# Optimization experiments

Hardware: AMD Instinct MI355X
Metric: run time of the kernel (lower is better)

The kernel has to match this reference:

```python
import jax, jax.numpy as jnp
import numpy as np

ALPHA = 0.15       # blend weight for merged mean vs center token
SIZE_DELTA = 0.0   # additive smoothing on cluster sizes


def setup_inputs() -> dict:
    key = jax.random.key(0)
    B, T, C = 8, 4096, 1024
    x = jax.random.normal(key, (B, T, C), dtype=jnp.float32)
    return {"x": x, "layer_idx": 0, "requested_r": 2048}


def reference(x, layer_idx, requested_r):
    B, T, C = x.shape
    K = max(1, T - int(requested_r))

    # token importance scores = squared L2 norm per token
    scores = jnp.sum(x * x, axis=-1)                      # [B, T]
    # CLS protection: force token 0 to be kept
    scores = scores.at[:, 0].set(jnp.finfo(scores.dtype).max)
    _, keep_idx = jax.lax.top_k(scores, K)                # [B, K]
    keep_idx = jnp.sort(keep_idx, axis=-1)

    # cosine nearest-kept-center assignment
    feat = x / (jnp.linalg.norm(x, axis=-1, keepdims=True) + 1e-12)  # [B, T, C]
    kept_feat = jnp.take_along_axis(feat, keep_idx[..., None], axis=1)  # [B, K, C]
    sim = jnp.einsum('bth,bkh->btk', feat, kept_feat)     # [B, T, K]
    assign_idx = jnp.argmax(sim, axis=-1)                 # [B, T]
    # force each kept center to self-assign (vectorized scatter,
    # replaces the original Python double for-loop with .item() syncs)
    b_idx = jnp.arange(B)[:, None]
    assign_idx = assign_idx.at[b_idx, keep_idx].set(jnp.arange(K)[None, :])

    # scatter-based size-weighted merge: segment mean over assigned tokens
    seg = (assign_idx + jnp.arange(B)[:, None] * K).reshape(-1)       # [B*T]
    sums = jax.ops.segment_sum(x.reshape(B * T, C), seg, num_segments=B * K)
    cnt = jax.ops.segment_sum(jnp.ones((B * T,), x.dtype), seg, num_segments=B * K)
    merged = (sums / (cnt[:, None] + SIZE_DELTA)).reshape(B, K, C)    # [B, K, C]

    x_kept = jnp.take_along_axis(x, keep_idx[..., None], axis=1)      # [B, K, C]
    out = (1.0 - ALPHA) * x_kept + ALPHA * merged
    return out
```

## Files before the change

kernel.cpp:

```cpp
#include <hip/hip_runtime.h>
#include <hip/hip_bf16.h>
#include <float.h>
#include <math.h>

constexpr int B_ = 8;
constexpr int T_ = 4096;
constexpr int C_ = 1024;
constexpr int K_ = 2048;
constexpr int MROWS = T_ - K_;

constexpr int BM = 128, BN = 128, BK = 32;
constexpr int NB = K_ / BN;
constexpr int NKS = C_ / BK;
constexpr float REFINE_DELTA = 4e-4f;

typedef _Float16 f16x8 __attribute__((ext_vector_type(8)));
typedef float    f32x4 __attribute__((ext_vector_type(4)));

__device__ __forceinline__ void gload16(const ushort* g, ushort* l) {
  __builtin_amdgcn_global_load_lds(
      (const __attribute__((address_space(1))) unsigned int*)g,
      (__attribute__((address_space(3))) unsigned int*)l, 16, 0, 0);
}

__global__ __launch_bounds__(256) void split_score_kernel(
    const float* __restrict__ x, ushort* __restrict__ xh,
    double* __restrict__ sd, float* __restrict__ rnorm)
{
  int lane = threadIdx.x & 63, wave = threadIdx.x >> 6;
  int row = blockIdx.x * 4 + wave;
  size_t base = (size_t)row * C_;
  double s = 0.0;
  #pragma unroll
  for (int j = 0; j < 4; j++) {
    int i4 = j * 256 + lane * 4;
    float4 v = *reinterpret_cast<const float4*>(&x[base + i4]);
    ushort4 h;
    { _Float16 a = (_Float16)v.x; h.x = *(ushort*)&a; }
    { _Float16 a = (_Float16)v.y; h.y = *(ushort*)&a; }
    { _Float16 a = (_Float16)v.z; h.z = *(ushort*)&a; }
    { _Float16 a = (_Float16)v.w; h.w = *(ushort*)&a; }
    *reinterpret_cast<ushort4*>(&xh[base + i4]) = h;
    s += (double)v.x * v.x + (double)v.y * v.y
       + (double)v.z * v.z + (double)v.w * v.w;
  }
  #pragma unroll
  for (int off = 32; off > 0; off >>= 1) s += __shfl_down(s, off);
  if (lane == 0) {
    sd[row] = s;
    rnorm[row] = (float)(1.0 / (sqrt(s) + 1e-12));
  }
}

__global__ __launch_bounds__(256) void rank_kernel(
    const double* __restrict__ sd, int* __restrict__ flag)
{
  int b = blockIdx.y;
  __shared__ double sh[T_];
  for (int i = threadIdx.x; i < T_; i += 256)
    sh[i] = (i == 0) ? DBL_MAX : sd[b * T_ + i];
  __syncthreads();
  int t = blockIdx.x * 128 + (threadIdx.x >> 1);
  int half = threadIdx.x & 1;
  double key = sh[t];
  int cnt = 0;
  int j0 = half * 2048;
  #pragma unroll 4
  for (int jj = 0; jj < 2048; jj++) {
    int j = j0 + jj;
    double sj = sh[j];
    cnt += (sj > key) || (sj == key && j < t);
  }
  cnt += __shfl_xor(cnt, 1);
  if (half == 0) flag[b * T_ + t] = (cnt < K_) ? 1 : 0;
}

__global__ __launch_bounds__(256) void select_kernel(
    const int* __restrict__ flag, int* __restrict__ keep_idx,
    int* __restrict__ drop_idx, int* __restrict__ assign)
{
  int b = blockIdx.x, tid = threadIdx.x;
  __shared__ int sums[256];
  int f[16], s = 0;
  int base = b * T_ + tid * 16;
  #pragma unroll
  for (int i = 0; i < 16; i++) { f[i] = flag[base + i]; s += f[i]; }
  sums[tid] = s;
  __syncthreads();
  for (int off = 1; off < 256; off <<= 1) {
    int v = 0;
    if (tid >= off) v = sums[tid - off];
    __syncthreads();
    if (tid >= off) sums[tid] += v;
    __syncthreads();
  }
  int run = (tid == 0) ? 0 : sums[tid - 1];
  #pragma unroll
  for (int i = 0; i < 16; i++) {
    int t = tid * 16 + i;
    if (f[i]) { keep_idx[b * K_ + run] = t; assign[b * T_ + t] = run; run++; }
    else drop_idx[b * MROWS + (t - run)] = t;
  }
}

__global__ void zero_kernel(int* __restrict__ cnt, int* __restrict__ nref)
{
  int i = blockIdx.x * 256 + threadIdx.x;
  if (i < B_ * K_) cnt[i] = 1;
  if (i == 0) *nref = 0;
}

__global__ __launch_bounds__(256) void mfma_argmax_kernel(
    const ushort* __restrict__ xh, const float* __restrict__ rnorm,
    const int* __restrict__ keep_idx, const int* __restrict__ drop_idx,
    float* __restrict__ pb, float* __restrict__ ps, int* __restrict__ pk)
{
  __shared__ __align__(16) ushort lds[3][2][4][128][8];

  int b  = blockIdx.z;
  int m0 = blockIdx.y * BM;
  int n0 = blockIdx.x * BN;
  int tid = threadIdx.x;
  int lane = tid & 63, wave = tid >> 6;
  int quad = lane >> 4, col = lane & 15;
  int wm = wave >> 1, wn = wave & 1;

  int srow = tid & 127;
  int sc8  = (tid >> 7) * 8;

  int dtok_s = drop_idx[b * MROWS + m0 + srow];
  const ushort* ga = xh + (size_t)(b * T_ + dtok_s) * C_;
  int ktok_s = keep_idx[b * K_ + n0 + srow];
  const ushort* gb = xh + (size_t)(b * T_ + ktok_s) * C_;

  int ldst = tid * 8;

  float scale[4]; int ncand[4];
  #pragma unroll
  for (int j = 0; j < 4; j++) {
    int nn = n0 + wn * 64 + j * 16 + col;
    ncand[j] = nn;
    scale[j] = rnorm[b * T_ + keep_idx[b * K_ + nn]];
  }

  f32x4 acc[4][4];
  #pragma unroll
  for (int i = 0; i < 4; i++)
    #pragma unroll
    for (int j = 0; j < 4; j++) acc[i][j] = (f32x4)0.f;

  auto issue = [&](int stg) {
    int k0 = stg * BK;
    ushort* base = &lds[stg % 3][0][0][0][0];
    gload16(ga + k0 + sc8,      base + ldst);
    gload16(ga + k0 + 16 + sc8, base + ldst + 2048);
    gload16(gb + k0 + sc8,      base + 4096 + ldst);
    gload16(gb + k0 + 16 + sc8, base + 4096 + ldst + 2048);
  };

  issue(0);
  issue(1);
  asm volatile("s_waitcnt vmcnt(4)" ::: "memory");
  __builtin_amdgcn_sched_barrier(0);
  __builtin_amdgcn_s_barrier();
  __builtin_amdgcn_sched_barrier(0);

  for (int ks = 0; ks < NKS; ks++) {
    int cur = ks % 3;
    if (ks <= NKS - 3) issue(ks + 2);

    f16x8 fa[4], fb[4];
    #pragma unroll
    for (int i = 0; i < 4; i++) {
      int row = wm * 64 + i * 16 + col;
      fa[i] = *reinterpret_cast<const f16x8*>(&lds[cur][0][quad][row][0]);
    }
    #pragma unroll
    for (int j = 0; j < 4; j++) {
      int row = wn * 64 + j * 16 + col;
      fb[j] = *reinterpret_cast<const f16x8*>(&lds[cur][1][quad][row][0]);
    }
    #pragma unroll
    for (int i = 0; i < 4; i++)
      #pragma unroll
      for (int j = 0; j < 4; j++)
        acc[i][j] = __builtin_amdgcn_mfma_f32_16x16x32_f16(fa[i], fb[j], acc[i][j], 0, 0, 0);

    if (ks <= NKS - 3) {
      asm volatile("s_waitcnt vmcnt(4)" ::: "memory");
    } else if (ks == NKS - 2) {
      asm volatile("s_waitcnt vmcnt(0)" ::: "memory");
    }
    __builtin_amdgcn_sched_barrier(0);
    if (ks < NKS - 1) {
      __builtin_amdgcn_s_barrier();
      __builtin_amdgcn_sched_barrier(0);
    }
  }

  float* redb   = (float*)(&lds[0][0][0][0][0]);
  float* redsec = redb + 256;
  int*   redk   = (int*)(redb + 512);

  #pragma unroll
  for (int i = 0; i < 4; i++) {
    #pragma unroll
    for (int r = 0; r < 4; r++) {
      float b1 = -FLT_MAX, b2 = -FLT_MAX; int k1 = 0;
      #pragma unroll
      for (int j = 0; j < 4; j++) {
        float v = acc[i][j][r] * scale[j];
        if (v > b1) { b2 = b1; b1 = v; k1 = ncand[j]; }
        else if (v > b2) b2 = v;
      }
      #pragma unroll
      for (int off = 1; off < 16; off <<= 1) {
        float ob1 = __shfl_xor(b1, off);
        float ob2 = __shfl_xor(b2, off);
        int   ok1 = __shfl_xor(k1, off);
        if (ob1 > b1 || (ob1 == b1 && ok1 < k1)) { b2 = fmaxf(b1, ob2); b1 = ob1; k1 = ok1; }
        else b2 = fmaxf(b2, ob1);
      }
      if (col == 0) {
        int tl = wm * 64 + i * 16 + quad * 4 + r;
        redb[wn * 128 + tl] = b1; redsec[wn * 128 + tl] = b2; redk[wn * 128 + tl] = k1;
      }
    }
  }
  __syncthreads();
  if (tid < 128) {
    float b1 = redb[tid], b2 = redsec[tid]; int k1 = redk[tid];
    float o1 = redb[128 + tid], o2 = redsec[128 + tid]; int ok = redk[128 + tid];
    if (o1 > b1) { b2 = fmaxf(b1, o2); b1 = o1; k1 = ok; }
    else b2 = fmaxf(b2, o1);
    size_t p = ((size_t)(b * NB + blockIdx.x)) * MROWS + m0 + tid;
    pb[p] = b1; ps[p] = b2; pk[p] = k1;
  }
}

__global__ __launch_bounds__(256) void reduce2_kernel(
    const float* __restrict__ pb, const float* __restrict__ ps, const int* __restrict__ pk,
    const float* __restrict__ rnorm, const int* __restrict__ drop_idx,
    int* __restrict__ assign, int* __restrict__ cnt,
    int* __restrict__ rlist, int* __restrict__ nref)
{
  int idx2 = blockIdx.x * 256 + threadIdx.x;
  int b = idx2 >> 11;
  int rc = idx2 & (MROWS - 1);
  float b1 = -FLT_MAX, b2 = -FLT_MAX; int k1 = 0;
  for (int nb = 0; nb < NB; nb++) {
    size_t p = ((size_t)(b * NB + nb)) * MROWS + rc;
    float v = pb[p], s = ps[p]; int k = pk[p];
    if (v > b1) { b2 = fmaxf(b1, s); b1 = v; k1 = k; }
    else b2 = fmaxf(b2, v);
  }
  int t = drop_idx[idx2];
  assign[b * T_ + t] = k1;
  atomicAdd(&cnt[b * K_ + k1], 1);
  if ((b1 - b2) * rnorm[b * T_ + t] < REFINE_DELTA) {
    int qi = atomicAdd(nref, 1);
    rlist[qi] = idx2;
  }
}

__global__ __launch_bounds__(256) void refine_kernel(
    const float* __restrict__ x, const double* __restrict__ sd,
    const int* __restrict__ keep_idx, const int* __restrict__ drop_idx,
    const float* __restrict__ rnorm,
    const float* __restrict__ pb, const float* __restrict__ ps, const int* __restrict__ pk,
    const int* __restrict__ nref, const int* __restrict__ rlist,
    int* __restrict__ assign, int* __restrict__ cnt)
{
  __shared__ __align__(16) float xs[C_];
  __shared__ int cand[K_];
  __shared__ int ncand_s;
  __shared__ double wv[4];
  __shared__ int wk[4];
  __shared__ float spb[NB], sps[NB];
  __shared__ int spk[NB];
  int n = *nref;
  int lane = threadIdx.x & 63, wave = threadIdx.x >> 6;
  for (int qi = blockIdx.x; qi < n; qi += gridDim.x) {
    int idx2 = rlist[qi];
    int b = idx2 >> 11, rc = idx2 & (MROWS - 1);
    int t = drop_idx[idx2];
    int bt = b * T_ + t;
    __syncthreads();
    const float* xt = x + ((size_t)b * T_ + t) * C_;
    for (int i = threadIdx.x; i < C_; i += 256) xs[i] = xt[i];
    if (threadIdx.x < NB) {
      size_t p = ((size_t)(b * NB + threadIdx.x)) * MROWS + rc;
      spb[threadIdx.x] = pb[p]; sps[threadIdx.x] = ps[p]; spk[threadIdx.x] = pk[p];
    }
    __syncthreads();
    if (threadIdx.x == 0) {
      float b1 = -FLT_MAX;
      for (int nb = 0; nb < NB; nb++) if (spb[nb] > b1) b1 = spb[nb];
      float thr = b1 - REFINE_DELTA / rnorm[bt];
      int nc = 0;
      for (int nb = 0; nb < NB; nb++) {
        if (spb[nb] >= thr) {
          if (sps[nb] >= thr) { for (int j = 0; j < BN; j++) cand[nc++] = nb * BN + j; }
          else cand[nc++] = spk[nb];
        }
      }
      ncand_s = nc;
    }
    __syncthreads();
    int nc = ncand_s;
    double bv = -DBL_MAX; int bk = 0x7fffffff;
    for (int ci = wave; ci < nc; ci += 4) {
      int k = cand[ci];
      int kt = keep_idx[b * K_ + k];
      const float* xr = x + ((size_t)b * T_ + kt) * C_;
      double s = 0.0;
      int c0 = lane * 16;
      #pragma unroll
      for (int c = 0; c < 16; c += 4) {
        float4 v = *reinterpret_cast<const float4*>(&xr[c0 + c]);
        s += (double)xs[c0 + c]     * v.x + (double)xs[c0 + c + 1] * v.y
           + (double)xs[c0 + c + 2] * v.z + (double)xs[c0 + c + 3] * v.w;
      }
      #pragma unroll
      for (int off = 32; off > 0; off >>= 1) s += __shfl_down(s, off);
      s = __shfl(s, 0);
      s /= sqrt(sd[b * T_ + kt]);
      if (s > bv || (s == bv && k < bk)) { bv = s; bk = k; }
    }
    if (lane == 0) { wv[wave] = bv; wk[wave] = bk; }
    __syncthreads();
    if (threadIdx.x == 0) {
      double fb = wv[0]; int fk = wk[0];
      for (int w2 = 1; w2 < 4; w2++)
        if (wv[w2] > fb || (wv[w2] == fb && wk[w2] < fk)) { fb = wv[w2]; fk = wk[w2]; }
      int old = assign[bt];
      if (fk != old) {
        atomicSub(&cnt[b * K_ + old], 1);
        atomicAdd(&cnt[b * K_ + fk], 1);
        assign[bt] = fk;
      }
    }
  }
}

__global__ __launch_bounds__(256) void scan_kernel(
    const int* __restrict__ cnt, int* __restrict__ offs, int* __restrict__ cursor)
{
  int b = blockIdx.x, tid = threadIdx.x;
  __shared__ int sums[256];
  int v[8], s = 0;
  int base = b * K_ + tid * 8;
  #pragma unroll
  for (int i = 0; i < 8; i++) { v[i] = cnt[base + i]; s += v[i]; }
  sums[tid] = s;
  __syncthreads();
  for (int off = 1; off < 256; off <<= 1) {
    int t2 = 0;
    if (tid >= off) t2 = sums[tid - off];
    __syncthreads();
    if (tid >= off) sums[tid] += t2;
    __syncthreads();
  }
  int run = (tid == 0) ? 0 : sums[tid - 1];
  #pragma unroll
  for (int i = 0; i < 8; i++) { offs[base + i] = run; cursor[base + i] = run; run += v[i]; }
}

__global__ void scatter_kernel(const int* __restrict__ assign,
                               int* __restrict__ cursor, int* __restrict__ lists)
{
  int i = blockIdx.x * 256 + threadIdx.x;
  int b = i >> 12, t = i & (T_ - 1);
  int p = atomicAdd(&cursor[b * K_ + assign[i]], 1);
  lists[b * T_ + p] = t;
}

__global__ __launch_bounds__(256) void merge_kernel(
    const float* __restrict__ x, const int* __restrict__ keep_idx,
    const int* __restrict__ cnt, const int* __restrict__ offs,
    const int* __restrict__ lists, float* __restrict__ out)
{
  __shared__ int toks[256];
  int b = blockIdx.y, k = blockIdx.x;
  int m = cnt[b * K_ + k], off = offs[b * K_ + k];
  const float* xb = x + (size_t)b * T_ * C_;
  int c4 = threadIdx.x * 4;
  float sx = 0.f, sy = 0.f, sz = 0.f, sw = 0.f;
  for (int basei = 0; basei < m; basei += 256) {
    int nchunk = min(256, m - basei);
    __syncthreads();
    if (threadIdx.x < nchunk) toks[threadIdx.x] = lists[b * T_ + off + basei + threadIdx.x];
    __syncthreads();
    for (int i = 0; i < nchunk; i++) {
      int tok = toks[i];
      float4 v = *reinterpret_cast<const float4*>(&xb[(size_t)tok * C_ + c4]);
      sx += v.x; sy += v.y; sz += v.z; sw += v.w;
    }
  }
  int kt = keep_idx[b * K_ + k];
  float4 xk = *reinterpret_cast<const float4*>(&xb[(size_t)kt * C_ + c4]);
  float fm = (float)m;
  float4 o;
  o.x = 0.85f * xk.x + 0.15f * (sx / fm);
  o.y = 0.85f * xk.y + 0.15f * (sy / fm);
  o.z = 0.85f * xk.z + 0.15f * (sz / fm);
  o.w = 0.85f * xk.w + 0.15f * (sw / fm);
  *reinterpret_cast<float4*>(&out[((size_t)b * K_ + k) * C_ + c4]) = o;
}

extern "C" void kernel_launch(void* const* d_in, const int* in_sizes, int n_in,
                              void* d_out, int out_size, void* d_ws, size_t ws_size,
                              hipStream_t stream)
{
  const float* x = (const float*)d_in[0];
  float* out = (float*)d_out;

  char* w = (char*)d_ws;
  ushort* xh    = (ushort*)w;  w += sizeof(ushort) * (size_t)B_ * T_ * C_;
  float* pb     = (float*)w;   w += sizeof(float) * (size_t)B_ * NB * MROWS;
  float* ps     = (float*)w;   w += sizeof(float) * (size_t)B_ * NB * MROWS;
  int*   pk     = (int*)w;     w += sizeof(int) * (size_t)B_ * NB * MROWS;
  double* sd    = (double*)w;  w += sizeof(double) * B_ * T_;
  float* rnorm  = (float*)w;   w += sizeof(float) * B_ * T_;
  int* flag     = (int*)w;     w += sizeof(int) * B_ * T_;
  int* keep_idx = (int*)w;     w += sizeof(int) * B_ * K_;
  int* drop_idx = (int*)w;     w += sizeof(int) * B_ * MROWS;
  int* assign   = (int*)w;     w += sizeof(int) * B_ * T_;
  int* cnt      = (int*)w;     w += sizeof(int) * B_ * K_;
  int* offs     = (int*)w;     w += sizeof(int) * B_ * K_;
  int* cursor   = (int*)w;     w += sizeof(int) * B_ * K_;
  int* lists    = (int*)w;     w += sizeof(int) * B_ * T_;
  int* rlist    = (int*)w;     w += sizeof(int) * B_ * MROWS;
  int* nref     = (int*)w;     w += 256;

  split_score_kernel<<<B_ * T_ / 4, 256, 0, stream>>>(x, xh, sd, rnorm);
  rank_kernel<<<dim3(T_ / 128, B_), 256, 0, stream>>>(sd, flag);
  select_kernel<<<B_, 256, 0, stream>>>(flag, keep_idx, drop_idx, assign);
  zero_kernel<<<(B_ * K_ + 255) / 256, 256, 0, stream>>>(cnt, nref);
  mfma_argmax_kernel<<<dim3(NB, MROWS / BM, B_), 256, 0, stream>>>(
      xh, rnorm, keep_idx, drop_idx, pb, ps, pk);
  reduce2_kernel<<<B_ * MROWS / 256, 256, 0, stream>>>(
      pb, ps, pk, rnorm, drop_idx, assign, cnt, rlist, nref);
  refine_kernel<<<256, 256, 0, stream>>>(
      x, sd, keep_idx, drop_idx, rnorm, pb, ps, pk, nref, rlist, assign, cnt);
  scan_kernel<<<B_, 256, 0, stream>>>(cnt, offs, cursor);
  scatter_kernel<<<B_ * T_ / 256, 256, 0, stream>>>(assign, cursor, lists);
  merge_kernel<<<dim3(K_, B_), 256, 0, stream>>>(x, keep_idx, cnt, offs, lists, out);
}
```

Before: 558.0 us.

## Enlarge MFMA argmax tiles to 256x256, spread rank work wider, fuse zero init

The similarity GEMM now uses 256x256x64 tiles, 512 threads and 8 waves, with double buffering in place of the triple buffer and manual waitcnt. Each wave computes 128x64 outputs, which gives more operand reuse per LDS load and halves the partial-argmax columns that reduce2 reads. The rank kernel now splits each token's comparison over 16 lanes to get more parallel blocks, and the zero init moves into select_kernel, removing one launch. Risks: double buffering with __syncthreads may expose load latency, higher register and LDS use cuts occupancy, and the grid shrinks to 8x8x8 = 512 blocks.

```diff
diff --git a/kernel.cpp b/kernel.cpp
--- a/kernel.cpp
+++ b/kernel.cpp
@@ -9,7 +9,7 @@
 constexpr int K_ = 2048;
 constexpr int MROWS = T_ - K_;
 
-constexpr int BM = 128, BN = 128, BK = 32;
+constexpr int BM = 256, BN = 256, BK = 64;
 constexpr int NB = K_ / BN;
 constexpr int NKS = C_ / BK;
 constexpr float REFINE_DELTA = 4e-4f;
@@ -60,24 +60,28 @@
   for (int i = threadIdx.x; i < T_; i += 256)
     sh[i] = (i == 0) ? DBL_MAX : sd[b * T_ + i];
   __syncthreads();
-  int t = blockIdx.x * 128 + (threadIdx.x >> 1);
-  int half = threadIdx.x & 1;
+  int tt = threadIdx.x >> 4;
+  int g  = threadIdx.x & 15;
+  int t  = blockIdx.x * 16 + tt;
   double key = sh[t];
   int cnt = 0;
-  int j0 = half * 2048;
   #pragma unroll 4
-  for (int jj = 0; jj < 2048; jj++) {
-    int j = j0 + jj;
+  for (int jj = 0; jj < 256; jj++) {
+    int j = jj * 16 + g;
     double sj = sh[j];
     cnt += (sj > key) || (sj == key && j < t);
   }
   cnt += __shfl_xor(cnt, 1);
-  if (half == 0) flag[b * T_ + t] = (cnt < K_) ? 1 : 0;
+  cnt += __shfl_xor(cnt, 2);
+  cnt += __shfl_xor(cnt, 4);
+  cnt += __shfl_xor(cnt, 8);
+  if (g == 0) flag[b * T_ + t] = (cnt < K_) ? 1 : 0;
 }
 
 __global__ __launch_bounds__(256) void select_kernel(
     const int* __restrict__ flag, int* __restrict__ keep_idx,
-    int* __restrict__ drop_idx, int* __restrict__ assign)
+    int* __restrict__ drop_idx, int* __restrict__ assign,
+    int* __restrict__ cnt, int* __restrict__ nref)
 {
   int b = blockIdx.x, tid = threadIdx.x;
   __shared__ int sums[256];
@@ -101,40 +105,34 @@
     if (f[i]) { keep_idx[b * K_ + run] = t; assign[b * T_ + t] = run; run++; }
     else drop_idx[b * MROWS + (t - run)] = t;
   }
-}
-
-__global__ void zero_kernel(int* __restrict__ cnt, int* __restrict__ nref)
-{
-  int i = blockIdx.x * 256 + threadIdx.x;
-  if (i < B_ * K_) cnt[i] = 1;
-  if (i == 0) *nref = 0;
-}
-
-__global__ __launch_bounds__(256) void mfma_argmax_kernel(
+  #pragma unroll
+  for (int i = 0; i < 8; i++) cnt[b * K_ + tid * 8 + i] = 1;
+  if (b == 0 && tid == 0) *nref = 0;
+}
+
+__global__ __launch_bounds__(512) void mfma_argmax_kernel(
     const ushort* __restrict__ xh, const float* __restrict__ rnorm,
     const int* __restrict__ keep_idx, const int* __restrict__ drop_idx,
     float* __restrict__ pb, float* __restrict__ ps, int* __restrict__ pk)
 {
-  __shared__ __align__(16) ushort lds[3][2][4][128][8];
+  __shared__ __align__(16) ushort lds[2][2][8][256][8];
 
   int b  = blockIdx.z;
   int m0 = blockIdx.y * BM;
   int n0 = blockIdx.x * BN;
   int tid = threadIdx.x;
-  int lane = tid & 63, wave = tid >> 6;
+  int lane = tid & 63, w = tid >> 6;
   int quad = lane >> 4, col = lane & 15;
-  int wm = wave >> 1, wn = wave & 1;
-
-  int srow = tid & 127;
-  int sc8  = (tid >> 7) * 8;
-
+  int wm = w >> 2, wn = w & 3;
+
+  int rg = w & 3;
+  int cb = (w >> 2) * 4;
+  int srow = rg * 64 + lane;
   int dtok_s = drop_idx[b * MROWS + m0 + srow];
   const ushort* ga = xh + (size_t)(b * T_ + dtok_s) * C_;
   int ktok_s = keep_idx[b * K_ + n0 + srow];
   const ushort* gb = xh + (size_t)(b * T_ + ktok_s) * C_;
 
-  int ldst = tid * 8;
-
   float scale[4]; int ncand[4];
   #pragma unroll
   for (int j = 0; j < 4; j++) {
@@ -143,67 +141,54 @@
     scale[j] = rnorm[b * T_ + keep_idx[b * K_ + nn]];
   }
 
-  f32x4 acc[4][4];
-  #pragma unroll
-  for (int i = 0; i < 4; i++)
+  f32x4 acc[8][4];
+  #pragma unroll
+  for (int i = 0; i < 8; i++)
     #pragma unroll
     for (int j = 0; j < 4; j++) acc[i][j] = (f32x4)0.f;
 
-  auto issue = [&](int stg) {
-    int k0 = stg * BK;
-    ushort* base = &lds[stg % 3][0][0][0][0];
-    gload16(ga + k0 + sc8,      base + ldst);
-    gload16(ga + k0 + 16 + sc8, base + ldst + 2048);
-    gload16(gb + k0 + sc8,      base + 4096 + ldst);
-    gload16(gb + k0 + 16 + sc8, base + 4096 + ldst + 2048);
+  auto issue = [&](int ks, int st) {
+    int k0 = ks * BK;
+    #pragma unroll
+    for (int c = 0; c < 4; c++) {
+      int ch = cb + c;
+      gload16(ga + k0 + ch * 8, &lds[st][0][ch][srow][0]);
+      gload16(gb + k0 + ch * 8, &lds[st][1][ch][srow][0]);
+    }
   };
 
-  issue(0);
-  issue(1);
-  asm volatile("s_waitcnt vmcnt(4)" ::: "memory");
-  __builtin_amdgcn_sched_barrier(0);
-  __builtin_amdgcn_s_barrier();
-  __builtin_amdgcn_sched_barrier(0);
+  issue(0, 0);
+  __syncthreads();
 
   for (int ks = 0; ks < NKS; ks++) {
-    int cur = ks % 3;
-    if (ks <= NKS - 3) issue(ks + 2);
-
-    f16x8 fa[4], fb[4];
+    int cur = ks & 1;
+    if (ks < NKS - 1) issue(ks + 1, cur ^ 1);
+
     #pragma unroll
-    for (int i = 0; i < 4; i++) {
-      int row = wm * 64 + i * 16 + col;
-      fa[i] = *reinterpret_cast<const f16x8*>(&lds[cur][0][quad][row][0]);
-    }
-    #pragma unroll
-    for (int j = 0; j < 4; j++) {
-      int row = wn * 64 + j * 16 + col;
-      fb[j] = *reinterpret_cast<const f16x8*>(&lds[cur][1][quad][row][0]);
-    }
-    #pragma unroll
-    for (int i = 0; i < 4; i++)
+    for (int s = 0; s < 2; s++) {
+      f16x8 fb[4];
       #pragma unroll
       for (int j = 0; j < 4; j++)
-        acc[i][j] = __builtin_amdgcn_mfma_f32_16x16x32_f16(fa[i], fb[j], acc[i][j], 0, 0, 0);
-
-    if (ks <= NKS - 3) {
-      asm volatile("s_waitcnt vmcnt(4)" ::: "memory");
-    } else if (ks == NKS - 2) {
-      asm volatile("s_waitcnt vmcnt(0)" ::: "memory");
-    }
-    __builtin_amdgcn_sched_barrier(0);
-    if (ks < NKS - 1) {
-      __builtin_amdgcn_s_barrier();
-      __builtin_amdgcn_sched_barrier(0);
-    }
+        fb[j] = *reinterpret_cast<const f16x8*>(
+            &lds[cur][1][s * 4 + quad][wn * 64 + j * 16 + col][0]);
+      #pragma unroll
+      for (int i = 0; i < 8; i++) {
+        f16x8 fa = *reinterpret_cast<const f16x8*>(
+            &lds[cur][0][s * 4 + quad][wm * 128 + i * 16 + col][0]);
+        #pragma unroll
+        for (int j = 0; j < 4; j++)
+          acc[i][j] = __builtin_amdgcn_mfma_f32_16x16x32_f16(fa, fb[j], acc[i][j], 0, 0, 0);
+      }
+    }
+    __syncthreads();
   }
 
   float* redb   = (float*)(&lds[0][0][0][0][0]);
-  float* redsec = redb + 256;
-  int*   redk   = (int*)(redb + 512);
-
-  #pragma unroll
-  for (int i = 0; i < 4; i++) {
+  float* redsec = redb + 1024;
+  int*   redk   = (int*)(redb + 2048);
+
+  #pragma unroll
+  for (int i = 0; i < 8; i++) {
     #pragma unroll
     for (int r = 0; r < 4; r++) {
       float b1 = -FLT_MAX, b2 = -FLT_MAX; int k1 = 0;
@@ -222,17 +207,20 @@
         else b2 = fmaxf(b2, ob1);
       }
       if (col == 0) {
-        int tl = wm * 64 + i * 16 + quad * 4 + r;
-        redb[wn * 128 + tl] = b1; redsec[wn * 128 + tl] = b2; redk[wn * 128 + tl] = k1;
+        int tl = wm * 128 + i * 16 + quad * 4 + r;
+        redb[wn * 256 + tl] = b1; redsec[wn * 256 + tl] = b2; redk[wn * 256 + tl] = k1;
       }
     }
   }
   __syncthreads();
-  if (tid < 128) {
+  if (tid < 256) {
     float b1 = redb[tid], b2 = redsec[tid]; int k1 = redk[tid];
-    float o1 = redb[128 + tid], o2 = redsec[128 + tid]; int ok = redk[128 + tid];
-    if (o1 > b1) { b2 = fmaxf(b1, o2); b1 = o1; k1 = ok; }
-    else b2 = fmaxf(b2, o1);
+    #pragma unroll
+    for (int q = 1; q < 4; q++) {
+      float o1 = redb[q * 256 + tid], o2 = redsec[q * 256 + tid]; int ok = redk[q * 256 + tid];
+      if (o1 > b1) { b2 = fmaxf(b1, o2); b1 = o1; k1 = ok; }
+      else b2 = fmaxf(b2, o1);
+    }
     size_t p = ((size_t)(b * NB + blockIdx.x)) * MROWS + m0 + tid;
     pb[p] = b1; ps[p] = b2; pk[p] = k1;
   }
@@ -434,10 +422,9 @@
   int* nref     = (int*)w;     w += 256;
 
   split_score_kernel<<<B_ * T_ / 4, 256, 0, stream>>>(x, xh, sd, rnorm);
-  rank_kernel<<<dim3(T_ / 128, B_), 256, 0, stream>>>(sd, flag);
-  select_kernel<<<B_, 256, 0, stream>>>(flag, keep_idx, drop_idx, assign);
-  zero_kernel<<<(B_ * K_ + 255) / 256, 256, 0, stream>>>(cnt, nref);
-  mfma_argmax_kernel<<<dim3(NB, MROWS / BM, B_), 256, 0, stream>>>(
+  rank_kernel<<<dim3(T_ / 16, B_), 256, 0, stream>>>(sd, flag);
+  select_kernel<<<B_, 256, 0, stream>>>(flag, keep_idx, drop_idx, assign, cnt, nref);
+  mfma_argmax_kernel<<<dim3(NB, MROWS / BM, B_), 512, 0, stream>>>(
       xh, rnorm, keep_idx, drop_idx, pb, ps, pk);
   reduce2_kernel<<<B_ * MROWS / 256, 256, 0, stream>>>(
       pb, ps, pk, rnorm, drop_idx, assign, cnt, rlist, nref);
```

Measured after the change: 675.3 us. 21.0% more time.

## Parallelize rank and refine per wave, fuse zero init, simplify GEMM pipeline

Applied to the files above, without the earlier changes.

The rank kernel now splits each token's comparison across 16 threads instead of 2, giving 8x more blocks. Zero initialisation of cluster counts moves into the select kernel, removing one launch. The MFMA argmax kernel goes from a triple-buffered, hand-synchronised pipeline to double buffering with __syncthreads. It also writes per-64-column partials directly, dropping the LDS cross-wave reduction and doubling the partial count. The refine kernel assigns one wave per ambiguous token, with register-held query rows, more blocks and no block barriers. The risks are a weaker load/compute overlap in the GEMM and extra partial-reduction traffic.

```diff
diff --git a/kernel.cpp b/kernel.cpp
--- a/kernel.cpp
+++ b/kernel.cpp
@@ -11,7 +11,7 @@
 
 constexpr int BM = 128, BN = 128, BK = 32;
 constexpr int NB = K_ / BN;
-constexpr int NKS = C_ / BK;
+constexpr int NG = K_ / 64;
 constexpr float REFINE_DELTA = 4e-4f;
 
 typedef _Float16 f16x8 __attribute__((ext_vector_type(8)));
@@ -60,24 +60,28 @@
   for (int i = threadIdx.x; i < T_; i += 256)
     sh[i] = (i == 0) ? DBL_MAX : sd[b * T_ + i];
   __syncthreads();
-  int t = blockIdx.x * 128 + (threadIdx.x >> 1);
-  int half = threadIdx.x & 1;
+  int tt = threadIdx.x >> 4;
+  int g  = threadIdx.x & 15;
+  int t  = blockIdx.x * 16 + tt;
   double key = sh[t];
   int cnt = 0;
-  int j0 = half * 2048;
   #pragma unroll 4
-  for (int jj = 0; jj < 2048; jj++) {
-    int j = j0 + jj;
+  for (int jj = 0; jj < 256; jj++) {
+    int j = jj * 16 + g;
     double sj = sh[j];
     cnt += (sj > key) || (sj == key && j < t);
   }
   cnt += __shfl_xor(cnt, 1);
-  if (half == 0) flag[b * T_ + t] = (cnt < K_) ? 1 : 0;
+  cnt += __shfl_xor(cnt, 2);
+  cnt += __shfl_xor(cnt, 4);
+  cnt += __shfl_xor(cnt, 8);
+  if (g == 0) flag[b * T_ + t] = (cnt < K_) ? 1 : 0;
 }
 
 __global__ __launch_bounds__(256) void select_kernel(
     const int* __restrict__ flag, int* __restrict__ keep_idx,
-    int* __restrict__ drop_idx, int* __restrict__ assign)
+    int* __restrict__ drop_idx, int* __restrict__ assign,
+    int* __restrict__ cnt, int* __restrict__ nref)
 {
   int b = blockIdx.x, tid = threadIdx.x;
   __shared__ int sums[256];
@@ -101,13 +105,9 @@
     if (f[i]) { keep_idx[b * K_ + run] = t; assign[b * T_ + t] = run; run++; }
     else drop_idx[b * MROWS + (t - run)] = t;
   }
-}
-
-__global__ void zero_kernel(int* __restrict__ cnt, int* __restrict__ nref)
-{
-  int i = blockIdx.x * 256 + threadIdx.x;
-  if (i < B_ * K_) cnt[i] = 1;
-  if (i == 0) *nref = 0;
+  #pragma unroll
+  for (int i = 0; i < 8; i++) cnt[b * K_ + tid * 8 + i] = 1;
+  if (b == 0 && tid == 0) *nref = 0;
 }
 
 __global__ __launch_bounds__(256) void mfma_argmax_kernel(
@@ -115,7 +115,7 @@
     const int* __restrict__ keep_idx, const int* __restrict__ drop_idx,
     float* __restrict__ pb, float* __restrict__ ps, int* __restrict__ pk)
 {
-  __shared__ __align__(16) ushort lds[3][2][4][128][8];
+  __shared__ __align__(16) ushort lds[2][2][4][128][8];
 
   int b  = blockIdx.z;
   int m0 = blockIdx.y * BM;
@@ -149,25 +149,20 @@
     #pragma unroll
     for (int j = 0; j < 4; j++) acc[i][j] = (f32x4)0.f;
 
-  auto issue = [&](int stg) {
-    int k0 = stg * BK;
-    ushort* base = &lds[stg % 3][0][0][0][0];
+  auto issue = [&](int k0, int st) {
+    ushort* base = &lds[st][0][0][0][0];
     gload16(ga + k0 + sc8,      base + ldst);
     gload16(ga + k0 + 16 + sc8, base + ldst + 2048);
     gload16(gb + k0 + sc8,      base + 4096 + ldst);
     gload16(gb + k0 + 16 + sc8, base + 4096 + ldst + 2048);
   };
 
-  issue(0);
-  issue(1);
-  asm volatile("s_waitcnt vmcnt(4)" ::: "memory");
-  __builtin_amdgcn_sched_barrier(0);
-  __builtin_amdgcn_s_barrier();
-  __builtin_amdgcn_sched_barrier(0);
-
-  for (int ks = 0; ks < NKS; ks++) {
-    int cur = ks % 3;
-    if (ks <= NKS - 3) issue(ks + 2);
+  issue(0, 0);
+  __syncthreads();
+
+  for (int ks = 0; ks < C_ / BK; ks++) {
+    int cur = ks & 1;
+    if (ks < C_ / BK - 1) issue((ks + 1) * BK, cur ^ 1);
 
     f16x8 fa[4], fb[4];
     #pragma unroll
@@ -185,23 +180,10 @@
       #pragma unroll
       for (int j = 0; j < 4; j++)
         acc[i][j] = __builtin_amdgcn_mfma_f32_16x16x32_f16(fa[i], fb[j], acc[i][j], 0, 0, 0);
-
-    if (ks <= NKS - 3) {
-      asm volatile("s_waitcnt vmcnt(4)" ::: "memory");
-    } else if (ks == NKS - 2) {
-      asm volatile("s_waitcnt vmcnt(0)" ::: "memory");
-    }
-    __builtin_amdgcn_sched_barrier(0);
-    if (ks < NKS - 1) {
-      __builtin_amdgcn_s_barrier();
-      __builtin_amdgcn_sched_barrier(0);
-    }
-  }
-
-  float* redb   = (float*)(&lds[0][0][0][0][0]);
-  float* redsec = redb + 256;
-  int*   redk   = (int*)(redb + 512);
-
+    __syncthreads();
+  }
+
+  int g = blockIdx.x * 2 + wn;
   #pragma unroll
   for (int i = 0; i < 4; i++) {
     #pragma unroll
@@ -223,18 +205,10 @@
       }
       if (col == 0) {
         int tl = wm * 64 + i * 16 + quad * 4 + r;
-        redb[wn * 128 + tl] = b1; redsec[wn * 128 + tl] = b2; redk[wn * 128 + tl] = k1;
+        size_t p = ((size_t)(b * NG + g)) * MROWS + m0 + tl;
+        pb[p] = b1; ps[p] = b2; pk[p] = k1;
       }
     }
-  }
-  __syncthreads();
-  if (tid < 128) {
-    float b1 = redb[tid], b2 = redsec[tid]; int k1 = redk[tid];
-    float o1 = redb[128 + tid], o2 = redsec[128 + tid]; int ok = redk[128 + tid];
-    if (o1 > b1) { b2 = fmaxf(b1, o2); b1 = o1; k1 = ok; }
-    else b2 = fmaxf(b2, o1);
-    size_t p = ((size_t)(b * NB + blockIdx.x)) * MROWS + m0 + tid;
-    pb[p] = b1; ps[p] = b2; pk[p] = k1;
   }
 }
 
@@ -248,8 +222,8 @@
   int b = idx2 >> 11;
   int rc = idx2 & (MROWS - 1);
   float b1 = -FLT_MAX, b2 = -FLT_MAX; int k1 = 0;
-  for (int nb = 0; nb < NB; nb++) {
-    size_t p = ((size_t)(b * NB + nb)) * MROWS + rc;
+  for (int gg = 0; gg < NG; gg++) {
+    size_t p = ((size_t)(b * NG + gg)) * MROWS + rc;
     float v = pb[p], s = ps[p]; int k = pk[p];
     if (v > b1) { b2 = fmaxf(b1, s); b1 = v; k1 = k; }
     else b2 = fmaxf(b2, v);
@@ -271,73 +245,62 @@
     const int* __restrict__ nref, const int* __restrict__ rlist,
     int* __restrict__ assign, int* __restrict__ cnt)
 {
-  __shared__ __align__(16) float xs[C_];
-  __shared__ int cand[K_];
-  __shared__ int ncand_s;
-  __shared__ double wv[4];
-  __shared__ int wk[4];
-  __shared__ float spb[NB], sps[NB];
-  __shared__ int spk[NB];
   int n = *nref;
-  int lane = threadIdx.x & 63, wave = threadIdx.x >> 6;
-  for (int qi = blockIdx.x; qi < n; qi += gridDim.x) {
+  int lane = threadIdx.x & 63;
+  int gwave = (blockIdx.x * blockDim.x + threadIdx.x) >> 6;
+  int nwaves = (gridDim.x * blockDim.x) >> 6;
+  for (int qi = gwave; qi < n; qi += nwaves) {
     int idx2 = rlist[qi];
     int b = idx2 >> 11, rc = idx2 & (MROWS - 1);
     int t = drop_idx[idx2];
     int bt = b * T_ + t;
-    __syncthreads();
-    const float* xt = x + ((size_t)b * T_ + t) * C_;
-    for (int i = threadIdx.x; i < C_; i += 256) xs[i] = xt[i];
-    if (threadIdx.x < NB) {
-      size_t p = ((size_t)(b * NB + threadIdx.x)) * MROWS + rc;
-      spb[threadIdx.x] = pb[p]; sps[threadIdx.x] = ps[p]; spk[threadIdx.x] = pk[p];
-    }
-    __syncthreads();
-    if (threadIdx.x == 0) {
-      float b1 = -FLT_MAX;
-      for (int nb = 0; nb < NB; nb++) if (spb[nb] > b1) b1 = spb[nb];
-      float thr = b1 - REFINE_DELTA / rnorm[bt];
-      int nc = 0;
-      for (int nb = 0; nb < NB; nb++) {
-        if (spb[nb] >= thr) {
-          if (sps[nb] >= thr) { for (int j = 0; j < BN; j++) cand[nc++] = nb * BN + j; }
-          else cand[nc++] = spk[nb];
-        }
+    const float* xt = x + (size_t)bt * C_;
+    const float4* xtv = reinterpret_cast<const float4*>(xt + lane * 16);
+    float4 a0 = xtv[0], a1 = xtv[1], a2 = xtv[2], a3 = xtv[3];
+    float pbg = -FLT_MAX, psg = -FLT_MAX; int pkg = 0;
+    if (lane < NG) {
+      size_t p = ((size_t)(b * NG + lane)) * MROWS + rc;
+      pbg = pb[p]; psg = ps[p]; pkg = pk[p];
+    }
+    float b1 = pbg;
+    #pragma unroll
+    for (int off = 32; off > 0; off >>= 1) b1 = fmaxf(b1, __shfl_xor(b1, off));
+    float thr = b1 - REFINE_DELTA / rnorm[bt];
+
+    double bv = -DBL_MAX; int bk = 0x7fffffff;
+    for (int g = 0; g < NG; g++) {
+      float gpb = __shfl(pbg, g);
+      if (gpb < thr) continue;
+      float gps = __shfl(psg, g);
+      int kfirst, kcount;
+      if (gps >= thr) { kfirst = g * 64; kcount = 64; }
+      else            { kfirst = __shfl(pkg, g); kcount = 1; }
+      for (int jj = 0; jj < kcount; jj++) {
+        int k = kfirst + jj;
+        int kt = keep_idx[b * K_ + k];
+        const float4* xrv = reinterpret_cast<const float4*>(
+            x + ((size_t)b * T_ + kt) * C_ + lane * 16);
+        float4 v0 = xrv[0], v1 = xrv[1], v2 = xrv[2], v3 = xrv[3];
+        double s = (double)a0.x * v0.x + (double)a0.y * v0.y
+                 + (double)a0.z * v0.z + (double)a0.w * v0.w
+                 + (double)a1.x * v1.x + (double)a1.y * v1.y
+                 + (double)a1.z * v1.z + (double)a1.w * v1.w
+                 + (double)a2.x * v2.x + (double)a2.y * v2.y
+                 + (double)a2.z * v2.z + (double)a2.w * v2.w
+                 + (double)a3.x * v3.x + (double)a3.y * v3.y
+                 + (double)a3.z * v3.z + (double)a3.w * v3.w;
+        #pragma unroll
+        for (int off = 32; off > 0; off >>= 1) s += __shfl_xor(s, off);
+        s /= sqrt(sd[b * T_ + kt]);
+        if (s > bv || (s == bv && k < bk)) { bv = s; bk = k; }
       }
-      ncand_s = nc;
-    }
-    __syncthreads();
-    int nc = ncand_s;
-    double bv = -DBL_MAX; int bk = 0x7fffffff;
-    for (int ci = wave; ci < nc; ci += 4) {
-      int k = cand[ci];
-      int kt = keep_idx[b * K_ + k];
-      const float* xr = x + ((size_t)b * T_ + kt) * C_;
-      double s = 0.0;
-      int c0 = lane * 16;
-      #pragma unroll
-      for (int c = 0; c < 16; c += 4) {
-        float4 v = *reinterpret_cast<const float4*>(&xr[c0 + c]);
-        s += (double)xs[c0 + c]     * v.x + (double)xs[c0 + c + 1] * v.y
-           + (double)xs[c0 + c + 2] * v.z + (double)xs[c0 + c + 3] * v.w;
-      }
-      #pragma unroll
-      for (int off = 32; off > 0; off >>= 1) s += __shfl_down(s, off);
-      s = __shfl(s, 0);
-      s /= sqrt(sd[b * T_ + kt]);
-      if (s > bv || (s == bv && k < bk)) { bv = s; bk = k; }
-    }
-    if (lane == 0) { wv[wave] = bv; wk[wave] = bk; }
-    __syncthreads();
-    if (threadIdx.x == 0) {
-      double fb = wv[0]; int fk = wk[0];
-      for (int w2 = 1; w2 < 4; w2++)
-        if (wv[w2] > fb || (wv[w2] == fb && wk[w2] < fk)) { fb = wv[w2]; fk = wk[w2]; }
+    }
+    if (lane == 0) {
       int old = assign[bt];
-      if (fk != old) {
+      if (bk != old) {
         atomicSub(&cnt[b * K_ + old], 1);
-        atomicAdd(&cnt[b * K_ + fk], 1);
-        assign[bt] = fk;
+        atomicAdd(&cnt[b * K_ + bk], 1);
+        assign[bt] = bk;
       }
     }
   }
@@ -417,9 +380,9 @@
 
   char* w = (char*)d_ws;
   ushort* xh    = (ushort*)w;  w += sizeof(ushort) * (size_t)B_ * T_ * C_;
-  float* pb     = (float*)w;   w += sizeof(float) * (size_t)B_ * NB * MROWS;
-  float* ps     = (float*)w;   w += sizeof(float) * (size_t)B_ * NB * MROWS;
-  int*   pk     = (int*)w;     w += sizeof(int) * (size_t)B_ * NB * MROWS;
+  float* pb     = (float*)w;   w += sizeof(float) * (size_t)B_ * NG * MROWS;
+  float* ps     = (float*)w;   w += sizeof(float) * (size_t)B_ * NG * MROWS;
+  int*   pk     = (int*)w;     w += sizeof(int) * (size_t)B_ * NG * MROWS;
   double* sd    = (double*)w;  w += sizeof(double) * B_ * T_;
   float* rnorm  = (float*)w;   w += sizeof(float) * B_ * T_;
   int* flag     = (int*)w;     w += sizeof(int) * B_ * T_;
@@ -434,14 +397,13 @@
   int* nref     = (int*)w;     w += 256;
 
   split_score_kernel<<<B_ * T_ / 4, 256, 0, stream>>>(x, xh, sd, rnorm);
-  rank_kernel<<<dim3(T_ / 128, B_), 256, 0, stream>>>(sd, flag);
-  select_kernel<<<B_, 256, 0, stream>>>(flag, keep_idx, drop_idx, assign);
-  zero_kernel<<<(B_ * K_ + 255) / 256, 256, 0, stream>>>(cnt, nref);
+  rank_kernel<<<dim3(T_ / 16, B_), 256, 0, stream>>>(sd, flag);
+  select_kernel<<<B_, 256, 0, stream>>>(flag, keep_idx, drop_idx, assign, cnt, nref);
   mfma_argmax_kernel<<<dim3(NB, MROWS / BM, B_), 256, 0, stream>>>(
       xh, rnorm, keep_idx, drop_idx, pb, ps, pk);
   reduce2_kernel<<<B_ * MROWS / 256, 256, 0, stream>>>(
       pb, ps, pk, rnorm, drop_idx, assign, cnt, rlist, nref);
-  refine_kernel<<<256, 256, 0, stream>>>(
+  refine_kernel<<<1024, 256, 0, stream>>>(
       x, sd, keep_idx, drop_idx, rnorm, pb, ps, pk, nref, rlist, assign, cnt);
   scan_kernel<<<B_, 256, 0, stream>>>(cnt, offs, cursor);
   scatter_kernel<<<B_ * T_ / 256, 256, 0, stream>>>(assign, cursor, lists);
```

Result: faster. 508.1 us (-8.9%).
